# Optimization experiments

Hardware: AMD Instinct MI355X
Metric: run time of the kernel (lower is better)

## Reference

```python
import jax, jax.numpy as jnp
import numpy as np

HIDDEN = 128
RHO = 5        # K // 2 with K = 10
J = 5
SCALE = 5.0


def setup_inputs() -> dict:
    key = jax.random.key(0)
    ks = jax.random.split(key, 16)
    B, N, D = 2, 4096, HIDDEN
    eigvs = jax.random.uniform(ks[0], (B, N, D), dtype=jnp.float32)  # eigenvalue encodings in [0,1)
    x = jax.random.normal(ks[1], (B, N, D), dtype=jnp.float32)
    U = jax.random.normal(ks[2], (B, N, N), dtype=jnp.float32) / np.sqrt(N)
    s = 1.0 / np.sqrt(D)
    return {
        "eigvs": eigvs, "x": x, "U": U,
        # Linear weights stored as [in, out] (already transposed vs torch)
        "Wa": jax.random.normal(ks[3], (D, RHO), dtype=jnp.float32) * s,
        "ba": jnp.zeros((RHO,), jnp.float32),
        "Wb": jax.random.normal(ks[4], (D, RHO), dtype=jnp.float32) * s,
        "bb": jnp.zeros((RHO,), jnp.float32),
        "Ws": jax.random.normal(ks[5], (D, J), dtype=jnp.float32) * s,
        "bs": jnp.zeros((J,), jnp.float32),
        "WS": jax.random.normal(ks[6], (D, D), dtype=jnp.float32) * s,
        "bS": jnp.zeros((D,), jnp.float32),
        "WM": jax.random.normal(ks[7], (J, D, D), dtype=jnp.float32) * s,
        "bM": jnp.zeros((J, D), jnp.float32),
        "Ww": jax.random.normal(ks[8], (D, D), dtype=jnp.float32) * s,
        "bw": jnp.zeros((D,), jnp.float32),
    }


def _generate_g(a, sx, rho):
    # a: [B, rho]; sx: [B, J, N, D] scaled eigenvalues. Even Chebyshev polys.
    T_odd = jnp.ones_like(sx)
    T_even = sx
    g = a[:, 0, None, None, None] * T_even
    for i in range(1, rho):
        T_odd = 2.0 * sx * T_even - T_odd
        T_even = 2.0 * sx * T_odd - T_even
        g = g + a[:, i, None, None, None] * T_even
    return g


def _generate_h(b, e, rho):
    # b: [B, rho]; e: [B, N, D]. Odd Chebyshev polys.
    T_odd = jnp.ones_like(e)
    T_even = e
    h = b[:, 0, None, None] * T_odd
    for i in range(1, rho):
        T_odd = 2.0 * e * T_even - T_odd
        T_even = 2.0 * e * T_odd - T_even
        h = h + b[:, i, None, None] * T_odd
    return h


def reference(eigvs, x, U, Wa, ba, Wb, bb, Ws, bs, WS, bS, WM, bM, Ww, bw):
    # Filter coefficients from pooled eigenvalue encodings
    a_tilde = (eigvs @ Wa + ba).mean(axis=-2)                      # [B, rho]
    b_tilde = (eigvs @ Wb + bb).mean(axis=-2)                      # [B, rho]
    scale_tilde = jax.nn.sigmoid((eigvs @ Ws + bs).mean(axis=-2)) * SCALE  # [B, J]

    h = _generate_h(b_tilde, eigvs, RHO)                           # [B, N, D] scaling filter
    sx = scale_tilde[:, :, None, None] * eigvs[:, None]            # [B, J, N, D]
    g = _generate_g(a_tilde, sx, RHO)                              # [B, J, N, D] wavelet filters

    # Spectral convolution: U diag(filter) U^T x, per channel
    xt = jnp.einsum('bmn,bmd->bnd', U, x)                          # U^T x
    y_h = jnp.einsum('bnm,bmd->bnd', U, h * xt)                    # [B, N, D]
    y_g = jnp.einsum('bnm,bjmd->bjnd', U, g * xt[:, None])         # [B, J, N, D]

    out = y_h @ WS + bS                                            # S_kernel
    out = out + jnp.einsum('bjnd,jde->bne', y_g, WM) + bM.sum(0)   # sum_j M_kernels[j]
    return out @ Ww + bw                                           # W
```

## Files before the change

### kernel.cpp

```cpp
#include <hip/hip_runtime.h>
#include <hip/hip_bf16.h>
#include <stdint.h>

typedef unsigned short u16;
typedef __attribute__((ext_vector_type(8))) short bf16x8;
typedef __attribute__((ext_vector_type(4))) float f32x4;
typedef __attribute__((ext_vector_type(4))) uint32_t u32x4;

__device__ inline u16 f2bf(float f) {
  union { float f; uint32_t u; } v; v.f = f;
  uint32_t u = v.u;
  u += 0x7FFFu + ((u >> 16) & 1u);
  return (u16)(u >> 16);
}

__device__ inline uint32_t pkbf(float a, float b) {
  union { __hip_bfloat162 h; uint32_t u; } c;
  c.h = __float22bfloat162_rn(float2{a, b});
  return c.u;
}

__device__ inline void gl_lds16(const void* g, void* s) {
  __builtin_amdgcn_global_load_lds(
      (const __attribute__((address_space(1))) void*)(uintptr_t)(g),
      (__attribute__((address_space(3))) void*)(uint32_t)(uintptr_t)(s),
      16, 0, 0);
}

__global__ __launch_bounds__(256) void k_pre(const float* __restrict__ eig,
                                             const float* __restrict__ x,
                                             float* __restrict__ part,
                                             u16* __restrict__ xT) {
  const int bid = blockIdx.x, t = threadIdx.x;
  if (bid < 64) {
    const int b = bid >> 5, chunk = bid & 31;
    const int d = t & 127, half = t >> 7;
    const float* p = eig + ((long)b * 4096 + chunk * 128 + half) * 128 + d;
    float s = 0.0f;
    for (int i = 0; i < 64; i++) s += p[(long)i * 256];
    __shared__ float red[256];
    red[t] = s;
    __syncthreads();
    if (t < 128) part[((long)b * 32 + chunk) * 128 + d] = red[t] + red[t + 128];
    return;
  }
  const int q = bid - 64;
  const int b = q >> 7, rem = q & 127;
  const int tr = rem & 63, tc = rem >> 6;
  const float* I = x + (long)b * 524288;
  u16* O = xT + (long)b * 524288;
  __shared__ uint32_t L[64][33];
  const int r = t >> 2, cq = (t & 3) * 4;
  const float* src = I + (long)(tr * 64 + r) * 128 + tc * 64;
#pragma unroll
  for (int i = 0; i < 4; i++) {
    const float4 f = *(const float4*)(src + cq + 16 * i);
    const int c = cq + 16 * i;
    L[r][(c >> 1)]     = pkbf(f.x, f.y);
    L[r][(c >> 1) + 1] = pkbf(f.z, f.w);
  }
  __syncthreads();
  const int r0 = (t & 7) * 8;
#pragma unroll
  for (int p = 0; p < 2; p++) {
    const int c = (t >> 3) + 32 * p;
    uint32_t w[4];
#pragma unroll
    for (int i = 0; i < 4; i++) {
      const uint32_t w0 = L[r0 + 2 * i][c >> 1];
      const uint32_t w1 = L[r0 + 2 * i + 1][c >> 1];
      const u16 v0 = (c & 1) ? (u16)(w0 >> 16) : (u16)(w0 & 0xffff);
      const u16 v1 = (c & 1) ? (u16)(w1 >> 16) : (u16)(w1 & 0xffff);
      w[i] = (uint32_t)v0 | ((uint32_t)v1 << 16);
    }
    u32x4* dst = (u32x4*)(O + (long)(tc * 64 + c) * 4096 + tr * 64 + r0);
    *dst = u32x4{w[0], w[1], w[2], w[3]};
  }
}

__global__ void k_foldcoeff(const float* __restrict__ WS, const float* __restrict__ WM,
                            const float* __restrict__ Ww, const float* __restrict__ bS,
                            const float* __restrict__ bM, const float* __restrict__ bw,
                            const float* __restrict__ part,
                            const float* __restrict__ Wa, const float* __restrict__ ba,
                            const float* __restrict__ Wb, const float* __restrict__ bb_,
                            const float* __restrict__ Ws, const float* __restrict__ bs,
                            u16* __restrict__ VT, float* __restrict__ cvec,
                            float* __restrict__ coeff) {
  const int q = blockIdx.x, e = threadIdx.x;
  if (q >= 769) {
    const int b = q - 769;
    __shared__ float sd[128];
    float s = 0.0f;
    for (int c = 0; c < 32; c++) s += part[((long)b * 32 + c) * 128 + e];
    sd[e] = s * (1.0f / 4096.0f);
    __syncthreads();
    if (e >= 15) return;
    const int kind = e / 5, r = e % 5;
    const float* W = (kind == 0) ? Wa : ((kind == 1) ? Wb : Ws);
    float v = 0.0f;
    for (int d = 0; d < 128; d++) v += sd[d] * W[d * 5 + r];
    v += (kind == 0) ? ba[r] : ((kind == 1) ? bb_[r] : bs[r]);
    if (kind == 2) v = 5.0f / (1.0f + __expf(-v));
    coeff[b * 16 + kind * 5 + r] = v;
    return;
  }
  if (q == 768) {
    float s = bw[e];
    for (int k = 0; k < 128; k++) {
      float t = bS[k];
#pragma unroll
      for (int j = 0; j < 5; j++) t += bM[j * 128 + k];
      s += t * Ww[k * 128 + e];
    }
    cvec[e] = s;
    return;
  }
  const int f = q >> 7, d = q & 127;
  const float* Frow = (f == 0) ? (WS + d * 128) : (WM + ((long)(f - 1) * 128 + d) * 128);
  float s = 0.0f;
  for (int k = 0; k < 128; k++) s += Frow[k] * Ww[k * 128 + e];
  VT[(long)e * 768 + f * 128 + d] = f2bf(s);
}

__global__ void k_filter(const float* __restrict__ eig, const float* __restrict__ xs,
                         const float* __restrict__ coeff, u16* __restrict__ Mod) {
  const int b = blockIdx.y;
  const int n = blockIdx.x * 2 + (threadIdx.x >> 7);
  const int d = threadIdx.x & 127;
  const long ridx = (long)b * 4096 + n;
  const long off = ridx * 128 + d;
  const float e = eig[off];
  float xv = 0.0f;
#pragma unroll
  for (int s = 0; s < 8; s++) xv += xs[off + (long)s * 1048576];
  const float* cf = coeff + b * 16;
  float To = 1.0f, Tev = e;
  float h = cf[5];
#pragma unroll
  for (int i = 1; i < 5; i++) {
    To = 2.0f * e * Tev - To;
    Tev = 2.0f * e * To - Tev;
    h += cf[5 + i] * To;
  }
  u16* row = Mod + ridx * 768;
  row[d] = f2bf(h * xv);
#pragma unroll
  for (int j = 0; j < 5; j++) {
    const float sx = cf[10 + j] * e;
    float To2 = 1.0f, Te2 = sx;
    float g = cf[0] * Te2;
#pragma unroll
    for (int i = 1; i < 5; i++) {
      To2 = 2.0f * sx * Te2 - To2;
      Te2 = 2.0f * sx * To2 - Te2;
      g += cf[i] * Te2;
    }
    row[(j + 1) * 128 + d] = f2bf(g * xv);
  }
}

__global__ void k_outred(const float* __restrict__ os, const float* __restrict__ cvec,
                         float* __restrict__ out) {
  const long i = (long)blockIdx.x * 256 + threadIdx.x;
  float4 r = *(const float4*)(os + 4 * i);
#pragma unroll
  for (int s = 1; s < 8; s++) {
    const float4 t = *(const float4*)(os + 4 * i + (long)s * 1048576);
    r.x += t.x; r.y += t.y; r.z += t.z; r.w += t.w;
  }
  const float4 cv = *(const float4*)(cvec + (i & 31) * 4);
  r.x += cv.x; r.y += cv.y; r.z += cv.z; r.w += cv.w;
  *(float4*)(out + 4 * i) = r;
}

template <int AT, int BT, int CT>
__global__ __launch_bounds__(256) void k_gemm(
    const void* __restrict__ A, long sA, int lda,
    const void* __restrict__ B, long sB, int ldb,
    void* __restrict__ C, long sC, int ldc, long kslice,
    int K, int kchunk, int m_tiles) {
  __shared__ __align__(16) u16 As[128 * 32];
  __shared__ __align__(16) u16 Bs[128 * 34 + 64];
  const int bb = blockIdx.z, ks = blockIdx.y;
  const int tm = blockIdx.x % m_tiles, tn = blockIdx.x / m_tiles;
  const int tid = threadIdx.x, wave = tid >> 6, lane = tid & 63;
  const int wm = (wave >> 1) * 64, wn = (wave & 1) * 64;
  f32x4 acc[4][4];
#pragma unroll
  for (int i = 0; i < 4; i++)
#pragma unroll
    for (int j = 0; j < 4; j++)
#pragma unroll
      for (int r = 0; r < 4; r++) acc[i][j][r] = 0.0f;
  const int a_off = (wm + (lane & 15)) * 64 + (lane >> 4) * 16;
  const int b_off = (BT == 2) ? ((wn + (lane & 15)) * 68 + (lane >> 4) * 16)
                              : ((wn + (lane & 15)) * 64 + (lane >> 4) * 16);
  const int b_nt_stride = (BT == 2) ? 1088 : 1024;
  const int srow = wave * 32 + (lane >> 2);
  const int scol = (lane & 3) * 8;
  for (int k0 = 0; k0 < kchunk; k0 += 32) {
    const int kb = ks * kchunk + k0;
    if constexpr (AT == 0) {
      const u16* Ab = (const u16*)A + (long)bb * sA + (long)tm * 128 * lda + kb;
#pragma unroll
      for (int i = 0; i < 2; i++)
        gl_lds16(Ab + (long)(srow + i * 16) * lda + scol,
                 (char*)As + (wave * 32 + i * 16) * 64);
    } else {
      const float* Af = (const float*)A + (long)bb * sA + (long)tm * 128 * lda + kb;
      const float* s0 = Af + (long)(tid >> 2) * lda + (tid & 3) * 8;
      const float4 f0 = *(const float4*)(s0);
      const float4 f1 = *(const float4*)(s0 + 4);
      *(u32x4*)((char*)As + tid * 16) =
          u32x4{pkbf(f0.x, f0.y), pkbf(f0.z, f0.w), pkbf(f1.x, f1.y), pkbf(f1.z, f1.w)};
      const float* s1 = s0 + (long)64 * lda;
      const float4 g0 = *(const float4*)(s1);
      const float4 g1 = *(const float4*)(s1 + 4);
      *(u32x4*)((char*)As + 4096 + tid * 16) =
          u32x4{pkbf(g0.x, g0.y), pkbf(g0.z, g0.w), pkbf(g1.x, g1.y), pkbf(g1.z, g1.w)};
    }
    if constexpr (BT == 0) {
      const u16* Bb = (const u16*)B + (long)bb * sB + (long)tn * 128 * ldb + kb;
#pragma unroll
      for (int i = 0; i < 2; i++)
        gl_lds16(Bb + (long)(srow + i * 16) * ldb + scol,
                 (char*)Bs + (wave * 32 + i * 16) * 64);
    } else {
      const int q = tid & 15, cb = tid >> 4;
      const float* r0 = (const float*)B + (long)bb * sB + (long)(kb + 2 * q) * ldb +
                        tn * 128 + cb * 8;
      const float* r1 = r0 + ldb;
      const float4 a0 = *(const float4*)(r0);
      const float4 a1 = *(const float4*)(r0 + 4);
      const float4 c0 = *(const float4*)(r1);
      const float4 c1 = *(const float4*)(r1 + 4);
      uint32_t* dw = (uint32_t*)Bs;
      const int base = (cb * 8) * 17 + q;
      dw[base + 0 * 17] = pkbf(a0.x, c0.x);
      dw[base + 1 * 17] = pkbf(a0.y, c0.y);
      dw[base + 2 * 17] = pkbf(a0.z, c0.z);
      dw[base + 3 * 17] = pkbf(a0.w, c0.w);
      dw[base + 4 * 17] = pkbf(a1.x, c1.x);
      dw[base + 5 * 17] = pkbf(a1.y, c1.y);
      dw[base + 6 * 17] = pkbf(a1.z, c1.z);
      dw[base + 7 * 17] = pkbf(a1.w, c1.w);
    }
    __syncthreads();
    bf16x8 af[4], bfr[4];
#pragma unroll
    for (int mt = 0; mt < 4; mt++)
      af[mt] = *(const bf16x8*)((const char*)As + a_off + mt * 1024);
#pragma unroll
    for (int nt = 0; nt < 4; nt++)
      bfr[nt] = *(const bf16x8*)((const char*)Bs + b_off + nt * b_nt_stride);
#pragma unroll
    for (int mt = 0; mt < 4; mt++)
#pragma unroll
      for (int nt = 0; nt < 4; nt++)
        acc[mt][nt] = __builtin_amdgcn_mfma_f32_16x16x32_bf16(af[mt], bfr[nt], acc[mt][nt], 0, 0, 0);
    __syncthreads();
  }
  const int lr = (lane >> 4) * 4, lc = lane & 15;
  if constexpr (CT == 1) {
    u16* Cb = (u16*)C + (long)bb * sC;
#pragma unroll
    for (int mt = 0; mt < 4; mt++)
#pragma unroll
      for (int nt = 0; nt < 4; nt++) {
        const int col = tn * 128 + wn + nt * 16 + lc;
#pragma unroll
        for (int r = 0; r < 4; r++) {
          const int row = tm * 128 + wm + mt * 16 + lr + r;
          Cb[(long)row * ldc + col] = f2bf(acc[mt][nt][r]);
        }
      }
  } else if constexpr (CT == 0) {
    float* Cf = (float*)C + (long)bb * sC + (long)ks * kslice;
#pragma unroll
    for (int mt = 0; mt < 4; mt++)
#pragma unroll
      for (int nt = 0; nt < 4; nt++) {
        const int col = tn * 128 + wn + nt * 16 + lc;
#pragma unroll
        for (int r = 0; r < 4; r++) {
          const int row = tm * 128 + wm + mt * 16 + lr + r;
          Cf[(long)row * ldc + col] = acc[mt][nt][r];
        }
      }
  } else {
    float* Cf = (float*)C + (long)bb * sC + (long)ks * kslice;
#pragma unroll
    for (int mt = 0; mt < 4; mt++)
#pragma unroll
      for (int nt = 0; nt < 4; nt++) {
        const int col = tn * 128 + wn + nt * 16 + lc;
#pragma unroll
        for (int r = 0; r < 4; r++) {
          const int row = tm * 128 + wm + mt * 16 + lr + r;
          Cf[(long)col * ldc + row] = acc[mt][nt][r];
        }
      }
  }
}

extern "C" void kernel_launch(void* const* d_in, const int* in_sizes, int n_in,
                              void* d_out, int out_size, void* d_ws, size_t ws_size,
                              hipStream_t stream) {
  const float* eig = (const float*)d_in[0];
  const float* x   = (const float*)d_in[1];
  const float* U   = (const float*)d_in[2];
  const float* Wa  = (const float*)d_in[3];
  const float* ba  = (const float*)d_in[4];
  const float* Wb  = (const float*)d_in[5];
  const float* bb  = (const float*)d_in[6];
  const float* Ws  = (const float*)d_in[7];
  const float* bs  = (const float*)d_in[8];
  const float* WSm = (const float*)d_in[9];
  const float* bS  = (const float*)d_in[10];
  const float* WM  = (const float*)d_in[11];
  const float* bM  = (const float*)d_in[12];
  const float* Ww  = (const float*)d_in[13];
  const float* bw  = (const float*)d_in[14];

  char* ws = (char*)d_ws;
  float* xs   = (float*)(ws + 0);
  float* os   = (float*)(ws + 0);
  u16*   Mod  = (u16*)(ws + 33554432);
  u16*   xT   = (u16*)(ws + 46137344);
  u16*   wT   = (u16*)(ws + 48234496);
  u16*   VT   = (u16*)(ws + 50331648);
  float* part = (float*)(ws + 50528256);
  float* coef = (float*)(ws + 50561024);
  float* cvec = (float*)(ws + 50561152);
  float* outp = (float*)d_out;

  if (ws_size < (size_t)50561664) return;

  k_pre<<<320, 256, 0, stream>>>(eig, x, part, xT);
  k_foldcoeff<<<771, 128, 0, stream>>>(WSm, WM, Ww, bS, bM, bw, part,
                                       Wa, ba, Wb, bb, Ws, bs, VT, cvec, coef);

  k_gemm<0, 2, 2><<<dim3(32, 8, 2), 256, 0, stream>>>(
      xT, 524288L, 4096, U, 16777216L, 4096,
      (void*)xs, 524288L, 128, 1048576L, 4096, 512, 1);

  k_filter<<<dim3(2048, 2), 256, 0, stream>>>(eig, xs, coef, Mod);

  k_gemm<0, 0, 1><<<dim3(32, 1, 2), 256, 0, stream>>>(
      VT, 0L, 768, Mod, 3145728L, 768,
      (void*)wT, 524288L, 4096, 0L, 768, 768, 1);

  k_gemm<1, 0, 0><<<dim3(32, 8, 2), 256, 0, stream>>>(
      U, 16777216L, 4096, wT, 524288L, 4096,
      (void*)os, 524288L, 128, 1048576L, 4096, 512, 32);

  k_outred<<<1024, 256, 0, stream>>>(os, cvec, outp);
}
```

Measured before the change: 312.8 us.

## Specialize GEMMs, prefetch U tiles, merge small kernels, store split-K partials in bf16

Replaces the templated GEMM with three specialized kernels. The two kernels that stream U register-prefetch the next fp32 tile while MFMAs run on the current one. The weight-folding kernel is merged into k_pre and the coefficient computation into an extra block column of the first GEMM, removing one launch. The split-K partials of the last GEMM are now stored in bf16 instead of fp32, halving reduction traffic at some cost in accuracy.

```diff
diff --git a/kernel.cpp b/kernel.cpp
--- a/kernel.cpp
+++ b/kernel.cpp
@@ -13,13 +13,14 @@
   u += 0x7FFFu + ((u >> 16) & 1u);
   return (u16)(u >> 16);
 }
-
 __device__ inline uint32_t pkbf(float a, float b) {
   union { __hip_bfloat162 h; uint32_t u; } c;
   c.h = __float22bfloat162_rn(float2{a, b});
   return c.u;
 }
-
+__device__ inline float bf2f(u16 h) {
+  union { uint32_t u; float f; } v; v.u = (uint32_t)h << 16; return v.f;
+}
 __device__ inline void gl_lds16(const void* g, void* s) {
   __builtin_amdgcn_global_load_lds(
       (const __attribute__((address_space(1))) void*)(uintptr_t)(g),
@@ -27,100 +28,189 @@
       16, 0, 0);
 }
 
-__global__ __launch_bounds__(256) void k_pre(const float* __restrict__ eig,
-                                             const float* __restrict__ x,
-                                             float* __restrict__ part,
-                                             u16* __restrict__ xT) {
+__global__ __launch_bounds__(256) void k_pre(
+    const float* __restrict__ eig, const float* __restrict__ x,
+    const float* __restrict__ WS, const float* __restrict__ WM,
+    const float* __restrict__ Ww, const float* __restrict__ bS,
+    const float* __restrict__ bM, const float* __restrict__ bw,
+    float* __restrict__ part, u16* __restrict__ xT,
+    u16* __restrict__ VT, float* __restrict__ cvec) {
   const int bid = blockIdx.x, t = threadIdx.x;
+  __shared__ float red[256];
+  __shared__ uint32_t L[64][33];
   if (bid < 64) {
     const int b = bid >> 5, chunk = bid & 31;
     const int d = t & 127, half = t >> 7;
     const float* p = eig + ((long)b * 4096 + chunk * 128 + half) * 128 + d;
     float s = 0.0f;
     for (int i = 0; i < 64; i++) s += p[(long)i * 256];
-    __shared__ float red[256];
     red[t] = s;
     __syncthreads();
     if (t < 128) part[((long)b * 32 + chunk) * 128 + d] = red[t] + red[t + 128];
     return;
   }
-  const int q = bid - 64;
-  const int b = q >> 7, rem = q & 127;
-  const int tr = rem & 63, tc = rem >> 6;
-  const float* I = x + (long)b * 524288;
-  u16* O = xT + (long)b * 524288;
-  __shared__ uint32_t L[64][33];
-  const int r = t >> 2, cq = (t & 3) * 4;
-  const float* src = I + (long)(tr * 64 + r) * 128 + tc * 64;
-#pragma unroll
-  for (int i = 0; i < 4; i++) {
-    const float4 f = *(const float4*)(src + cq + 16 * i);
-    const int c = cq + 16 * i;
-    L[r][(c >> 1)]     = pkbf(f.x, f.y);
-    L[r][(c >> 1) + 1] = pkbf(f.z, f.w);
-  }
-  __syncthreads();
-  const int r0 = (t & 7) * 8;
-#pragma unroll
-  for (int p = 0; p < 2; p++) {
-    const int c = (t >> 3) + 32 * p;
-    uint32_t w[4];
+  if (bid < 320) {
+    const int q = bid - 64;
+    const int b = q >> 7, rem = q & 127;
+    const int tr = rem & 63, tc = rem >> 6;
+    const float* I = x + (long)b * 524288;
+    u16* O = xT + (long)b * 524288;
+    const int r = t >> 2, cq = (t & 3) * 4;
+    const float* src = I + (long)(tr * 64 + r) * 128 + tc * 64;
 #pragma unroll
     for (int i = 0; i < 4; i++) {
-      const uint32_t w0 = L[r0 + 2 * i][c >> 1];
-      const uint32_t w1 = L[r0 + 2 * i + 1][c >> 1];
-      const u16 v0 = (c & 1) ? (u16)(w0 >> 16) : (u16)(w0 & 0xffff);
-      const u16 v1 = (c & 1) ? (u16)(w1 >> 16) : (u16)(w1 & 0xffff);
-      w[i] = (uint32_t)v0 | ((uint32_t)v1 << 16);
-    }
-    u32x4* dst = (u32x4*)(O + (long)(tc * 64 + c) * 4096 + tr * 64 + r0);
-    *dst = u32x4{w[0], w[1], w[2], w[3]};
-  }
-}
-
-__global__ void k_foldcoeff(const float* __restrict__ WS, const float* __restrict__ WM,
-                            const float* __restrict__ Ww, const float* __restrict__ bS,
-                            const float* __restrict__ bM, const float* __restrict__ bw,
-                            const float* __restrict__ part,
-                            const float* __restrict__ Wa, const float* __restrict__ ba,
-                            const float* __restrict__ Wb, const float* __restrict__ bb_,
-                            const float* __restrict__ Ws, const float* __restrict__ bs,
-                            u16* __restrict__ VT, float* __restrict__ cvec,
-                            float* __restrict__ coeff) {
-  const int q = blockIdx.x, e = threadIdx.x;
-  if (q >= 769) {
-    const int b = q - 769;
-    __shared__ float sd[128];
+      const float4 f = *(const float4*)(src + cq + 16 * i);
+      const int c = cq + 16 * i;
+      L[r][(c >> 1)]     = pkbf(f.x, f.y);
+      L[r][(c >> 1) + 1] = pkbf(f.z, f.w);
+    }
+    __syncthreads();
+    const int r0 = (t & 7) * 8;
+#pragma unroll
+    for (int p = 0; p < 2; p++) {
+      const int c = (t >> 3) + 32 * p;
+      uint32_t w[4];
+#pragma unroll
+      for (int i = 0; i < 4; i++) {
+        const uint32_t w0 = L[r0 + 2 * i][c >> 1];
+        const uint32_t w1 = L[r0 + 2 * i + 1][c >> 1];
+        const u16 v0 = (c & 1) ? (u16)(w0 >> 16) : (u16)(w0 & 0xffff);
+        const u16 v1 = (c & 1) ? (u16)(w1 >> 16) : (u16)(w1 & 0xffff);
+        w[i] = (uint32_t)v0 | ((uint32_t)v1 << 16);
+      }
+      u32x4* dst = (u32x4*)(O + (long)(tc * 64 + c) * 4096 + tr * 64 + r0);
+      *dst = u32x4{w[0], w[1], w[2], w[3]};
+    }
+    return;
+  }
+  if (bid < 704) {
+    const int q = (bid - 320) * 2 + (t >> 7);
+    const int e = t & 127;
+    const int f = q >> 7, d = q & 127;
+    const float* Frow = (f == 0) ? (WS + d * 128) : (WM + ((long)(f - 1) * 128 + d) * 128);
     float s = 0.0f;
-    for (int c = 0; c < 32; c++) s += part[((long)b * 32 + c) * 128 + e];
-    sd[e] = s * (1.0f / 4096.0f);
-    __syncthreads();
-    if (e >= 15) return;
-    const int kind = e / 5, r = e % 5;
+    for (int k = 0; k < 128; k++) s += Frow[k] * Ww[k * 128 + e];
+    VT[(long)e * 768 + f * 128 + d] = f2bf(s);
+    return;
+  }
+  if (t >= 128) return;
+  float s = bw[t];
+  for (int k = 0; k < 128; k++) {
+    float tv = bS[k];
+#pragma unroll
+    for (int j = 0; j < 5; j++) tv += bM[j * 128 + k];
+    s += tv * Ww[k * 128 + t];
+  }
+  cvec[t] = s;
+}
+
+__global__ __launch_bounds__(256) void k_gemm1(
+    const u16* __restrict__ xT, const float* __restrict__ U,
+    const float* __restrict__ part,
+    const float* __restrict__ Wa, const float* __restrict__ ba,
+    const float* __restrict__ Wb, const float* __restrict__ bb_,
+    const float* __restrict__ Ws, const float* __restrict__ bs,
+    float* __restrict__ xs, float* __restrict__ coeff) {
+  const int tn = blockIdx.x, ks = blockIdx.y, bb = blockIdx.z;
+  const int tid = threadIdx.x;
+  __shared__ float sd[128];
+  __shared__ __align__(16) u16 As[128 * 32];
+  __shared__ __align__(16) u16 Bs[128 * 34 + 64];
+  if (tn == 32) {
+    if (ks != 0) return;
+    if (tid < 128) {
+      float s = 0.0f;
+      for (int c = 0; c < 32; c++) s += part[((long)bb * 32 + c) * 128 + tid];
+      sd[tid] = s * (1.0f / 4096.0f);
+    }
+    __syncthreads();
+    if (tid >= 15) return;
+    const int kind = tid / 5, r = tid % 5;
     const float* W = (kind == 0) ? Wa : ((kind == 1) ? Wb : Ws);
     float v = 0.0f;
     for (int d = 0; d < 128; d++) v += sd[d] * W[d * 5 + r];
     v += (kind == 0) ? ba[r] : ((kind == 1) ? bb_[r] : bs[r]);
     if (kind == 2) v = 5.0f / (1.0f + __expf(-v));
-    coeff[b * 16 + kind * 5 + r] = v;
+    coeff[bb * 16 + kind * 5 + r] = v;
     return;
   }
-  if (q == 768) {
-    float s = bw[e];
-    for (int k = 0; k < 128; k++) {
-      float t = bS[k];
-#pragma unroll
-      for (int j = 0; j < 5; j++) t += bM[j * 128 + k];
-      s += t * Ww[k * 128 + e];
-    }
-    cvec[e] = s;
-    return;
-  }
-  const int f = q >> 7, d = q & 127;
-  const float* Frow = (f == 0) ? (WS + d * 128) : (WM + ((long)(f - 1) * 128 + d) * 128);
-  float s = 0.0f;
-  for (int k = 0; k < 128; k++) s += Frow[k] * Ww[k * 128 + e];
-  VT[(long)e * 768 + f * 128 + d] = f2bf(s);
+  const int wave = tid >> 6, lane = tid & 63;
+  const int wm = (wave >> 1) * 64, wn = (wave & 1) * 64;
+  f32x4 acc[4][4];
+#pragma unroll
+  for (int i = 0; i < 4; i++)
+#pragma unroll
+    for (int j = 0; j < 4; j++)
+#pragma unroll
+      for (int r = 0; r < 4; r++) acc[i][j][r] = 0.0f;
+  const int a_off = (wm + (lane & 15)) * 64 + (lane >> 4) * 16;
+  const int b_off = (wn + (lane & 15)) * 68 + (lane >> 4) * 16;
+  const int srow = wave * 32 + (lane >> 2);
+  const int scol = (lane & 3) * 8;
+  const u16* Ab = xT + (long)bb * 524288 + ks * 512;
+  const int q = tid & 15, cb = tid >> 4;
+  const float* Bbase = U + (long)bb * 16777216 + tn * 128 + cb * 8;
+  float4 ca0, ca1, cc0, cc1;
+  {
+    const float* r0 = Bbase + (long)(ks * 512 + 2 * q) * 4096;
+    ca0 = *(const float4*)(r0); ca1 = *(const float4*)(r0 + 4);
+    const float* r1 = r0 + 4096;
+    cc0 = *(const float4*)(r1); cc1 = *(const float4*)(r1 + 4);
+  }
+  for (int k0 = 0; k0 < 512; k0 += 32) {
+#pragma unroll
+    for (int i = 0; i < 2; i++)
+      gl_lds16(Ab + (long)(srow + i * 16) * 4096 + k0 + scol,
+               (char*)As + (wave * 32 + i * 16) * 64);
+    {
+      uint32_t* dw = (uint32_t*)Bs;
+      const int base = (cb * 8) * 17 + q;
+      dw[base + 0 * 17] = pkbf(ca0.x, cc0.x);
+      dw[base + 1 * 17] = pkbf(ca0.y, cc0.y);
+      dw[base + 2 * 17] = pkbf(ca0.z, cc0.z);
+      dw[base + 3 * 17] = pkbf(ca0.w, cc0.w);
+      dw[base + 4 * 17] = pkbf(ca1.x, cc1.x);
+      dw[base + 5 * 17] = pkbf(ca1.y, cc1.y);
+      dw[base + 6 * 17] = pkbf(ca1.z, cc1.z);
+      dw[base + 7 * 17] = pkbf(ca1.w, cc1.w);
+    }
+    __syncthreads();
+    const int kn = (k0 + 32 < 512) ? (k0 + 32) : k0;
+    float4 na0, na1, nc0, nc1;
+    {
+      const float* r0 = Bbase + (long)(ks * 512 + kn + 2 * q) * 4096;
+      na0 = *(const float4*)(r0); na1 = *(const float4*)(r0 + 4);
+      const float* r1 = r0 + 4096;
+      nc0 = *(const float4*)(r1); nc1 = *(const float4*)(r1 + 4);
+    }
+    bf16x8 af[4], bfr[4];
+#pragma unroll
+    for (int mt = 0; mt < 4; mt++)
+      af[mt] = *(const bf16x8*)((const char*)As + a_off + mt * 1024);
+#pragma unroll
+    for (int nt = 0; nt < 4; nt++)
+      bfr[nt] = *(const bf16x8*)((const char*)Bs + b_off + nt * 1088);
+#pragma unroll
+    for (int mt = 0; mt < 4; mt++)
+#pragma unroll
+      for (int nt = 0; nt < 4; nt++)
+        acc[mt][nt] = __builtin_amdgcn_mfma_f32_16x16x32_bf16(af[mt], bfr[nt], acc[mt][nt], 0, 0, 0);
+    __syncthreads();
+    ca0 = na0; ca1 = na1; cc0 = nc0; cc1 = nc1;
+  }
+  const int lr = (lane >> 4) * 4, lc = lane & 15;
+  float* Cf = xs + (long)bb * 524288 + (long)ks * 1048576;
+#pragma unroll
+  for (int mt = 0; mt < 4; mt++)
+#pragma unroll
+    for (int nt = 0; nt < 4; nt++) {
+      const int col = tn * 128 + wn + nt * 16 + lc;
+#pragma unroll
+      for (int r = 0; r < 4; r++) {
+        const int row = wm + mt * 16 + lr + r;
+        Cf[(long)col * 128 + row] = acc[mt][nt][r];
+      }
+    }
 }
 
 __global__ void k_filter(const float* __restrict__ eig, const float* __restrict__ xs,
@@ -160,30 +250,11 @@
   }
 }
 
-__global__ void k_outred(const float* __restrict__ os, const float* __restrict__ cvec,
-                         float* __restrict__ out) {
-  const long i = (long)blockIdx.x * 256 + threadIdx.x;
-  float4 r = *(const float4*)(os + 4 * i);
-#pragma unroll
-  for (int s = 1; s < 8; s++) {
-    const float4 t = *(const float4*)(os + 4 * i + (long)s * 1048576);
-    r.x += t.x; r.y += t.y; r.z += t.z; r.w += t.w;
-  }
-  const float4 cv = *(const float4*)(cvec + (i & 31) * 4);
-  r.x += cv.x; r.y += cv.y; r.z += cv.z; r.w += cv.w;
-  *(float4*)(out + 4 * i) = r;
-}
-
-template <int AT, int BT, int CT>
-__global__ __launch_bounds__(256) void k_gemm(
-    const void* __restrict__ A, long sA, int lda,
-    const void* __restrict__ B, long sB, int ldb,
-    void* __restrict__ C, long sC, int ldc, long kslice,
-    int K, int kchunk, int m_tiles) {
+__global__ __launch_bounds__(256) void k_gemm2(
+    const u16* __restrict__ VT, const u16* __restrict__ Mod, u16* __restrict__ wT) {
+  const int tn = blockIdx.x, bb = blockIdx.z;
   __shared__ __align__(16) u16 As[128 * 32];
-  __shared__ __align__(16) u16 Bs[128 * 34 + 64];
-  const int bb = blockIdx.z, ks = blockIdx.y;
-  const int tm = blockIdx.x % m_tiles, tn = blockIdx.x / m_tiles;
+  __shared__ __align__(16) u16 Bs[128 * 32];
   const int tid = threadIdx.x, wave = tid >> 6, lane = tid & 63;
   const int wm = (wave >> 1) * 64, wn = (wave & 1) * 64;
   f32x4 acc[4][4];
@@ -194,57 +265,17 @@
 #pragma unroll
       for (int r = 0; r < 4; r++) acc[i][j][r] = 0.0f;
   const int a_off = (wm + (lane & 15)) * 64 + (lane >> 4) * 16;
-  const int b_off = (BT == 2) ? ((wn + (lane & 15)) * 68 + (lane >> 4) * 16)
-                              : ((wn + (lane & 15)) * 64 + (lane >> 4) * 16);
-  const int b_nt_stride = (BT == 2) ? 1088 : 1024;
+  const int b_off = (wn + (lane & 15)) * 64 + (lane >> 4) * 16;
   const int srow = wave * 32 + (lane >> 2);
   const int scol = (lane & 3) * 8;
-  for (int k0 = 0; k0 < kchunk; k0 += 32) {
-    const int kb = ks * kchunk + k0;
-    if constexpr (AT == 0) {
-      const u16* Ab = (const u16*)A + (long)bb * sA + (long)tm * 128 * lda + kb;
-#pragma unroll
-      for (int i = 0; i < 2; i++)
-        gl_lds16(Ab + (long)(srow + i * 16) * lda + scol,
-                 (char*)As + (wave * 32 + i * 16) * 64);
-    } else {
-      const float* Af = (const float*)A + (long)bb * sA + (long)tm * 128 * lda + kb;
-      const float* s0 = Af + (long)(tid >> 2) * lda + (tid & 3) * 8;
-      const float4 f0 = *(const float4*)(s0);
-      const float4 f1 = *(const float4*)(s0 + 4);
-      *(u32x4*)((char*)As + tid * 16) =
-          u32x4{pkbf(f0.x, f0.y), pkbf(f0.z, f0.w), pkbf(f1.x, f1.y), pkbf(f1.z, f1.w)};
-      const float* s1 = s0 + (long)64 * lda;
-      const float4 g0 = *(const float4*)(s1);
-      const float4 g1 = *(const float4*)(s1 + 4);
-      *(u32x4*)((char*)As + 4096 + tid * 16) =
-          u32x4{pkbf(g0.x, g0.y), pkbf(g0.z, g0.w), pkbf(g1.x, g1.y), pkbf(g1.z, g1.w)};
-    }
-    if constexpr (BT == 0) {
-      const u16* Bb = (const u16*)B + (long)bb * sB + (long)tn * 128 * ldb + kb;
-#pragma unroll
-      for (int i = 0; i < 2; i++)
-        gl_lds16(Bb + (long)(srow + i * 16) * ldb + scol,
-                 (char*)Bs + (wave * 32 + i * 16) * 64);
-    } else {
-      const int q = tid & 15, cb = tid >> 4;
-      const float* r0 = (const float*)B + (long)bb * sB + (long)(kb + 2 * q) * ldb +
-                        tn * 128 + cb * 8;
-      const float* r1 = r0 + ldb;
-      const float4 a0 = *(const float4*)(r0);
-      const float4 a1 = *(const float4*)(r0 + 4);
-      const float4 c0 = *(const float4*)(r1);
-      const float4 c1 = *(const float4*)(r1 + 4);
-      uint32_t* dw = (uint32_t*)Bs;
-      const int base = (cb * 8) * 17 + q;
-      dw[base + 0 * 17] = pkbf(a0.x, c0.x);
-      dw[base + 1 * 17] = pkbf(a0.y, c0.y);
-      dw[base + 2 * 17] = pkbf(a0.z, c0.z);
-      dw[base + 3 * 17] = pkbf(a0.w, c0.w);
-      dw[base + 4 * 17] = pkbf(a1.x, c1.x);
-      dw[base + 5 * 17] = pkbf(a1.y, c1.y);
-      dw[base + 6 * 17] = pkbf(a1.z, c1.z);
-      dw[base + 7 * 17] = pkbf(a1.w, c1.w);
+  const u16* Bb = Mod + (long)bb * 3145728 + (long)tn * 128 * 768;
+  for (int k0 = 0; k0 < 768; k0 += 32) {
+#pragma unroll
+    for (int i = 0; i < 2; i++) {
+      gl_lds16(VT + (long)(srow + i * 16) * 768 + k0 + scol,
+               (char*)As + (wave * 32 + i * 16) * 64);
+      gl_lds16(Bb + (long)(srow + i * 16) * 768 + k0 + scol,
+               (char*)Bs + (wave * 32 + i * 16) * 64);
     }
     __syncthreads();
     bf16x8 af[4], bfr[4];
@@ -253,7 +284,7 @@
       af[mt] = *(const bf16x8*)((const char*)As + a_off + mt * 1024);
 #pragma unroll
     for (int nt = 0; nt < 4; nt++)
-      bfr[nt] = *(const bf16x8*)((const char*)Bs + b_off + nt * b_nt_stride);
+      bfr[nt] = *(const bf16x8*)((const char*)Bs + b_off + nt * 1024);
 #pragma unroll
     for (int mt = 0; mt < 4; mt++)
 #pragma unroll
@@ -262,46 +293,112 @@
     __syncthreads();
   }
   const int lr = (lane >> 4) * 4, lc = lane & 15;
-  if constexpr (CT == 1) {
-    u16* Cb = (u16*)C + (long)bb * sC;
-#pragma unroll
-    for (int mt = 0; mt < 4; mt++)
-#pragma unroll
-      for (int nt = 0; nt < 4; nt++) {
-        const int col = tn * 128 + wn + nt * 16 + lc;
-#pragma unroll
-        for (int r = 0; r < 4; r++) {
-          const int row = tm * 128 + wm + mt * 16 + lr + r;
-          Cb[(long)row * ldc + col] = f2bf(acc[mt][nt][r]);
-        }
+  u16* Cb = wT + (long)bb * 524288;
+#pragma unroll
+  for (int mt = 0; mt < 4; mt++)
+#pragma unroll
+    for (int nt = 0; nt < 4; nt++) {
+      const int col = tn * 128 + wn + nt * 16 + lc;
+#pragma unroll
+      for (int r = 0; r < 4; r++) {
+        const int row = wm + mt * 16 + lr + r;
+        Cb[(long)row * 4096 + col] = f2bf(acc[mt][nt][r]);
       }
-  } else if constexpr (CT == 0) {
-    float* Cf = (float*)C + (long)bb * sC + (long)ks * kslice;
-#pragma unroll
-    for (int mt = 0; mt < 4; mt++)
-#pragma unroll
-      for (int nt = 0; nt < 4; nt++) {
-        const int col = tn * 128 + wn + nt * 16 + lc;
-#pragma unroll
-        for (int r = 0; r < 4; r++) {
-          const int row = tm * 128 + wm + mt * 16 + lr + r;
-          Cf[(long)row * ldc + col] = acc[mt][nt][r];
-        }
+    }
+}
+
+__global__ __launch_bounds__(256) void k_gemm3(
+    const float* __restrict__ U, const u16* __restrict__ wT, u16* __restrict__ os16) {
+  const int tm = blockIdx.x, ks = blockIdx.y, bb = blockIdx.z;
+  __shared__ __align__(16) u16 As[128 * 32];
+  __shared__ __align__(16) u16 Bs[128 * 32];
+  const int tid = threadIdx.x, wave = tid >> 6, lane = tid & 63;
+  const int wm = (wave >> 1) * 64, wn = (wave & 1) * 64;
+  f32x4 acc[4][4];
+#pragma unroll
+  for (int i = 0; i < 4; i++)
+#pragma unroll
+    for (int j = 0; j < 4; j++)
+#pragma unroll
+      for (int r = 0; r < 4; r++) acc[i][j][r] = 0.0f;
+  const int a_off = (wm + (lane & 15)) * 64 + (lane >> 4) * 16;
+  const int b_off = (wn + (lane & 15)) * 64 + (lane >> 4) * 16;
+  const int srow = wave * 32 + (lane >> 2);
+  const int scol = (lane & 3) * 8;
+  const float* Abase = U + (long)bb * 16777216 +
+                       (long)(tm * 128 + (tid >> 2)) * 4096 + (tid & 3) * 8;
+  const u16* Bb = wT + (long)bb * 524288 + ks * 512;
+  float4 cf0, cf1, cg0, cg1;
+  {
+    const float* s0 = Abase + ks * 512;
+    cf0 = *(const float4*)(s0); cf1 = *(const float4*)(s0 + 4);
+    const float* s1 = s0 + 262144;
+    cg0 = *(const float4*)(s1); cg1 = *(const float4*)(s1 + 4);
+  }
+  for (int k0 = 0; k0 < 512; k0 += 32) {
+#pragma unroll
+    for (int i = 0; i < 2; i++)
+      gl_lds16(Bb + (long)(srow + i * 16) * 4096 + k0 + scol,
+               (char*)Bs + (wave * 32 + i * 16) * 64);
+    *(u32x4*)((char*)As + tid * 16) =
+        u32x4{pkbf(cf0.x, cf0.y), pkbf(cf0.z, cf0.w), pkbf(cf1.x, cf1.y), pkbf(cf1.z, cf1.w)};
+    *(u32x4*)((char*)As + 4096 + tid * 16) =
+        u32x4{pkbf(cg0.x, cg0.y), pkbf(cg0.z, cg0.w), pkbf(cg1.x, cg1.y), pkbf(cg1.z, cg1.w)};
+    __syncthreads();
+    const int kn = (k0 + 32 < 512) ? (k0 + 32) : k0;
+    float4 nf0, nf1, ng0, ng1;
+    {
+      const float* s0 = Abase + ks * 512 + kn;
+      nf0 = *(const float4*)(s0); nf1 = *(const float4*)(s0 + 4);
+      const float* s1 = s0 + 262144;
+      ng0 = *(const float4*)(s1); ng1 = *(const float4*)(s1 + 4);
+    }
+    bf16x8 af[4], bfr[4];
+#pragma unroll
+    for (int mt = 0; mt < 4; mt++)
+      af[mt] = *(const bf16x8*)((const char*)As + a_off + mt * 1024);
+#pragma unroll
+    for (int nt = 0; nt < 4; nt++)
+      bfr[nt] = *(const bf16x8*)((const char*)Bs + b_off + nt * 1024);
+#pragma unroll
+    for (int mt = 0; mt < 4; mt++)
+#pragma unroll
+      for (int nt = 0; nt < 4; nt++)
+        acc[mt][nt] = __builtin_amdgcn_mfma_f32_16x16x32_bf16(af[mt], bfr[nt], acc[mt][nt], 0, 0, 0);
+    __syncthreads();
+    cf0 = nf0; cf1 = nf1; cg0 = ng0; cg1 = ng1;
+  }
+  const int lr = (lane >> 4) * 4, lc = lane & 15;
+  u16* Cb = os16 + (long)ks * 1048576 + (long)bb * 524288;
+#pragma unroll
+  for (int mt = 0; mt < 4; mt++)
+#pragma unroll
+    for (int nt = 0; nt < 4; nt++) {
+      const int col = wn + nt * 16 + lc;
+#pragma unroll
+      for (int r = 0; r < 4; r++) {
+        const int row = tm * 128 + wm + mt * 16 + lr + r;
+        Cb[(long)row * 128 + col] = f2bf(acc[mt][nt][r]);
       }
-  } else {
-    float* Cf = (float*)C + (long)bb * sC + (long)ks * kslice;
-#pragma unroll
-    for (int mt = 0; mt < 4; mt++)
-#pragma unroll
-      for (int nt = 0; nt < 4; nt++) {
-        const int col = tn * 128 + wn + nt * 16 + lc;
-#pragma unroll
-        for (int r = 0; r < 4; r++) {
-          const int row = tm * 128 + wm + mt * 16 + lr + r;
-          Cf[(long)col * ldc + row] = acc[mt][nt][r];
-        }
-      }
-  }
+    }
+}
+
+__global__ void k_outred(const u16* __restrict__ os16, const float* __restrict__ cvec,
+                         float* __restrict__ out) {
+  const long i = (long)blockIdx.x * 256 + threadIdx.x;
+  const long j4 = i * 4;
+  float4 r = {0.0f, 0.0f, 0.0f, 0.0f};
+#pragma unroll
+  for (int s = 0; s < 8; s++) {
+    const uint2 v = *(const uint2*)(os16 + j4 + (long)s * 1048576);
+    r.x += bf2f((u16)(v.x & 0xffff));
+    r.y += bf2f((u16)(v.x >> 16));
+    r.z += bf2f((u16)(v.y & 0xffff));
+    r.w += bf2f((u16)(v.y >> 16));
+  }
+  const float4 cv = *(const float4*)(cvec + (i & 31) * 4);
+  r.x += cv.x; r.y += cv.y; r.z += cv.z; r.w += cv.w;
+  *(float4*)(out + j4) = r;
 }
 
 extern "C" void kernel_launch(void* const* d_in, const int* in_sizes, int n_in,
@@ -325,7 +422,7 @@
 
   char* ws = (char*)d_ws;
   float* xs   = (float*)(ws + 0);
-  float* os   = (float*)(ws + 0);
+  u16*   os16 = (u16*)(ws + 0);
   u16*   Mod  = (u16*)(ws + 33554432);
   u16*   xT   = (u16*)(ws + 46137344);
   u16*   wT   = (u16*)(ws + 48234496);
@@ -337,23 +434,15 @@
 
   if (ws_size < (size_t)50561664) return;
 
-  k_pre<<<320, 256, 0, stream>>>(eig, x, part, xT);
-  k_foldcoeff<<<771, 128, 0, stream>>>(WSm, WM, Ww, bS, bM, bw, part,
-                                       Wa, ba, Wb, bb, Ws, bs, VT, cvec, coef);
-
-  k_gemm<0, 2, 2><<<dim3(32, 8, 2), 256, 0, stream>>>(
-      xT, 524288L, 4096, U, 16777216L, 4096,
-      (void*)xs, 524288L, 128, 1048576L, 4096, 512, 1);
+  k_pre<<<705, 256, 0, stream>>>(eig, x, WSm, WM, Ww, bS, bM, bw, part, xT, VT, cvec);
+
+  k_gemm1<<<dim3(33, 8, 2), 256, 0, stream>>>(xT, U, part, Wa, ba, Wb, bb, Ws, bs, xs, coef);
 
   k_filter<<<dim3(2048, 2), 256, 0, stream>>>(eig, xs, coef, Mod);
 
-  k_gemm<0, 0, 1><<<dim3(32, 1, 2), 256, 0, stream>>>(
-      VT, 0L, 768, Mod, 3145728L, 768,
-      (void*)wT, 524288L, 4096, 0L, 768, 768, 1);
-
-  k_gemm<1, 0, 0><<<dim3(32, 8, 2), 256, 0, stream>>>(
-      U, 16777216L, 4096, wT, 524288L, 4096,
-      (void*)os, 524288L, 128, 1048576L, 4096, 512, 32);
-
-  k_outred<<<1024, 256, 0, stream>>>(os, cvec, outp);
-}
+  k_gemm2<<<dim3(32, 1, 2), 256, 0, stream>>>(VT, Mod, wT);
+
+  k_gemm3<<<dim3(32, 8, 2), 256, 0, stream>>>(U, wT, os16);
+
+  k_outred<<<1024, 256, 0, stream>>>(os16, cvec, outp);
+}
```

Result: faster. 293.9 us (-6.1%).
